# Optimization experiments

Hardware: AMD Instinct MI355X
Metric: run time of the kernel (lower is better)

Reference implementation:

```python
import jax, jax.numpy as jnp
import numpy as np

D_MODEL = 1024
D_STATE = 16
EXPANSION = 2
GROUPS = 16
D_INNER = EXPANSION * D_MODEL          # 2048
GROUP_SIZE = D_INNER // GROUPS         # 128
B, T = 2, 1024


def _rmsnorm(x, g, eps=1e-6):
    return x * jax.lax.rsqrt(jnp.mean(x * x, axis=-1, keepdims=True) + eps) * g


def setup_inputs() -> dict:
    key = jax.random.key(0)
    ks = jax.random.split(key, 8)
    s_in = 1.0 / np.sqrt(D_MODEL)
    s_inner = 1.0 / np.sqrt(D_INNER)
    s_ff = 1.0 / np.sqrt(4 * D_MODEL)
    return {
        "x": jax.random.normal(ks[0], (B, T, D_MODEL), dtype=jnp.float32),
        "A_log": jnp.log(jnp.linspace(1.0, float(D_STATE), D_STATE)).astype(jnp.float32),
        "g1": jnp.ones((D_MODEL,), jnp.float32),
        "g2": jnp.ones((D_MODEL,), jnp.float32),
        "W_in": jax.random.normal(ks[1], (2 * D_INNER, D_MODEL), jnp.float32) * s_in,
        "W_param": jax.random.normal(ks[2], (GROUPS * (1 + 2 * D_STATE), D_INNER), jnp.float32) * s_inner,
        "W_out": jax.random.normal(ks[3], (D_MODEL, D_INNER), jnp.float32) * s_inner,
        "W_ffn1": jax.random.normal(ks[4], (4 * D_MODEL, D_MODEL), jnp.float32) * s_in,
        "b_ffn1": jnp.zeros((4 * D_MODEL,), jnp.float32),
        "W_ffn2": jax.random.normal(ks[5], (D_MODEL, 4 * D_MODEL), jnp.float32) * s_ff,
        "b_ffn2": jnp.zeros((D_MODEL,), jnp.float32),
    }


def _ssm(u, delta, b, c, A_log):
    # u,delta: [B,T,D]; b,c: [B,T,D,N]. Sequential recurrence equivalent to
    # the module's chunked cumprod/cumsum formulation.
    A = -jnp.exp(A_log)                                   # [N]
    deltaA = jnp.clip(delta[..., None] * A, -10.0, 10.0)  # [B,T,D,N]
    expA = jnp.exp(deltaA)
    frac_exact = (expA - 1.0) / (A + 1e-12)
    frac = jnp.where(jnp.abs(deltaA) < 1e-4, delta[..., None], frac_exact)
    Bu = frac * (b * u[..., None])                        # [B,T,D,N]

    def step(h, inp):
        Ah_t, Bu_t, c_t = inp                             # [B,D,N] each
        h = Ah_t * h + Bu_t
        return h, jnp.sum(h * c_t, axis=-1)               # y_t: [B,D]

    tm = lambda a: jnp.moveaxis(a, 1, 0)                  # time-major [T,B,D,N]
    h0 = jnp.zeros(u.shape[:1] + u.shape[2:] + (A.shape[0],), u.dtype)
    _, ys = jax.lax.scan(step, h0, (tm(expA), tm(Bu), tm(c)))
    return jnp.moveaxis(ys, 0, 1)                         # [B,T,D]


def reference(x, A_log, g1, g2, W_in, W_param, W_out, W_ffn1, b_ffn1, W_ffn2, b_ffn2):
    Bsz, Tlen, _ = x.shape
    z = _rmsnorm(x, g1)
    xz_gate = jnp.einsum('btd,ed->bte', z, W_in)          # [B,T,2*D_inner]
    xz, gate = jnp.split(xz_gate, 2, axis=-1)
    xz = jax.nn.silu(xz)

    params = jnp.einsum('btd,pd->btp', xz, W_param)
    params = params.reshape(Bsz, Tlen, GROUPS, 1 + 2 * D_STATE)
    delta_g = params[..., :1]                             # [B,T,G,1]
    b_g = params[..., 1:1 + D_STATE]                      # [B,T,G,N]
    c_g = params[..., 1 + D_STATE:]                       # [B,T,G,N]
    delta = jax.nn.softplus(jnp.repeat(delta_g[..., 0], GROUP_SIZE, axis=2))  # [B,T,D_inner]
    b = jnp.repeat(b_g, GROUP_SIZE, axis=2)               # [B,T,D_inner,N]
    c = jnp.repeat(c_g, GROUP_SIZE, axis=2)

    y_ssm = _ssm(xz, delta, b, c, A_log)                  # [B,T,D_inner]
    y = y_ssm * jax.nn.silu(gate)
    y = jnp.einsum('bte,de->btd', y, W_out)
    x = x + y                                             # residual (dropout/droppath = identity in eval)

    h2 = _rmsnorm(x, g2)
    ffn = jnp.einsum('btf,df->btd',
                     jax.nn.silu(jnp.einsum('btd,fd->btf', h2, W_ffn1) + b_ffn1),
                     W_ffn2) + b_ffn2
    return x + ffn
```

## Files before the change

### kernel.cpp

```cpp
#include <hip/hip_runtime.h>
#include <hip/hip_bf16.h>
#include <stdint.h>

#define ROWS 2048
#define DM   1024
#define DI   2048
#define PPAD 640

typedef __bf16 bf16_t;
typedef __attribute__((ext_vector_type(8))) __bf16 bf16x8;
typedef __attribute__((ext_vector_type(4))) __bf16 bf16x4;
typedef __attribute__((ext_vector_type(4))) float f32x4;
typedef __attribute__((address_space(1))) void gvoid_t;
typedef __attribute__((address_space(3))) void lvoid_t;

#define G_IN   1048576ll
#define G_PAR  327680ll
#define G_OUT  524288ll
#define G_F1   1048576ll
#define G_F2   1048576ll
#define CVT_BLOCKS 15616
__global__ __launch_bounds__(256) void prep0(const float* __restrict__ W_in,
                                             const float* __restrict__ W_param,
                                             const float* __restrict__ W_out,
                                             const float* __restrict__ W_f1,
                                             const float* __restrict__ W_f2,
                                             bf16_t* o_in, bf16_t* o_par,
                                             bf16_t* o_out, bf16_t* o_f1,
                                             bf16_t* o_f2,
                                             const float* __restrict__ x,
                                             const float* __restrict__ g1,
                                             bf16_t* __restrict__ zb) {
  if (blockIdx.x >= CVT_BLOCKS) {
    int row = blockIdx.x - CVT_BLOCKS;
    int tid = threadIdx.x;
    const float4 v = *(const float4*)(x + (int64_t)row * DM + tid * 4);
    float ss = v.x * v.x + v.y * v.y + v.z * v.z + v.w * v.w;
#pragma unroll
    for (int o = 32; o; o >>= 1) ss += __shfl_xor(ss, o, 64);
    __shared__ float red[4];
    if ((tid & 63) == 0) red[tid >> 6] = ss;
    __syncthreads();
    float tot = red[0] + red[1] + red[2] + red[3];
    float sc = rsqrtf(tot * (1.0f / DM) + 1e-6f);
    const float4 gv = *(const float4*)(g1 + tid * 4);
    bf16_t* o = zb + (int64_t)row * DM + tid * 4;
    o[0] = (bf16_t)(v.x * sc * gv.x);
    o[1] = (bf16_t)(v.y * sc * gv.y);
    o[2] = (bf16_t)(v.z * sc * gv.z);
    o[3] = (bf16_t)(v.w * sc * gv.w);
    return;
  }
  int64_t g4 = (int64_t)blockIdx.x * 256 + threadIdx.x;
  const float* src; bf16_t* dst; int64_t e;
  if (g4 < G_IN) { e = g4 * 4; src = W_in; dst = o_in; }
  else if (g4 < G_IN + G_PAR) {
    e = (g4 - G_IN) * 4;
    int row = (int)(e >> 11), col = (int)(e & 2047);
    float4 v = make_float4(0.f, 0.f, 0.f, 0.f);
    if (row < 528) v = *(const float4*)(W_param + (int64_t)row * 2048 + col);
    bf16_t* o = o_par + e;
    o[0] = (bf16_t)v.x; o[1] = (bf16_t)v.y; o[2] = (bf16_t)v.z; o[3] = (bf16_t)v.w;
    return;
  }
  else if (g4 < G_IN + G_PAR + G_OUT) { e = (g4 - G_IN - G_PAR) * 4; src = W_out; dst = o_out; }
  else if (g4 < G_IN + G_PAR + G_OUT + G_F1) { e = (g4 - G_IN - G_PAR - G_OUT) * 4; src = W_f1; dst = o_f1; }
  else { e = (g4 - G_IN - G_PAR - G_OUT - G_F1) * 4; src = W_f2; dst = o_f2; }
  float4 v = *(const float4*)(src + e);
  bf16_t* o = dst + e;
  o[0] = (bf16_t)v.x; o[1] = (bf16_t)v.y; o[2] = (bf16_t)v.z; o[3] = (bf16_t)v.w;
}

__global__ __launch_bounds__(256) void rmsnorm_k(const float* __restrict__ x,
                                                 const float* __restrict__ g,
                                                 bf16_t* __restrict__ out) {
  int row = blockIdx.x;
  int tid = threadIdx.x;
  const float4 v = *(const float4*)(x + (int64_t)row * DM + tid * 4);
  float ss = v.x * v.x + v.y * v.y + v.z * v.z + v.w * v.w;
#pragma unroll
  for (int o = 32; o; o >>= 1) ss += __shfl_xor(ss, o, 64);
  __shared__ float red[4];
  if ((tid & 63) == 0) red[tid >> 6] = ss;
  __syncthreads();
  float tot = red[0] + red[1] + red[2] + red[3];
  float sc = rsqrtf(tot * (1.0f / DM) + 1e-6f);
  const float4 gv = *(const float4*)(g + tid * 4);
  bf16_t* o = out + (int64_t)row * DM + tid * 4;
  o[0] = (bf16_t)(v.x * sc * gv.x);
  o[1] = (bf16_t)(v.y * sc * gv.y);
  o[2] = (bf16_t)(v.z * sc * gv.z);
  o[3] = (bf16_t)(v.w * sc * gv.w);
}

__global__ __launch_bounds__(256) void silu_cvt(const float* __restrict__ in,
                                                bf16_t* __restrict__ out,
                                                int in_stride, int ncols) {
  int64_t e = ((int64_t)blockIdx.x * 256 + threadIdx.x) * 4;
  int row = (int)(e / ncols);
  int col = (int)(e % ncols);
  const float4 v = *(const float4*)(in + (int64_t)row * in_stride + col);
  bf16_t* o = out + e;
  o[0] = (bf16_t)(v.x / (1.f + expf(-v.x)));
  o[1] = (bf16_t)(v.y / (1.f + expf(-v.y)));
  o[2] = (bf16_t)(v.z / (1.f + expf(-v.z)));
  o[3] = (bf16_t)(v.w / (1.f + expf(-v.w)));
}

template <typename T>
__global__ __launch_bounds__(256) void ssm_prep(const T* __restrict__ params,
                                                const float* __restrict__ A_log,
                                                float* __restrict__ ssmp, int nparts) {
  int gid = blockIdx.x * 256 + threadIdx.x;
  int bg = gid >> 10, t = gid & 1023;
  int b = bg >> 4, g = bg & 15;
  float acc[33];
#pragma unroll
  for (int i = 0; i < 33; ++i) acc[i] = 0.f;
  for (int p = 0; p < nparts; ++p) {
    const T* pr = params + (int64_t)p * ROWS * PPAD + (int64_t)(b * 1024 + t) * PPAD + g * 33;
#pragma unroll
    for (int i = 0; i < 33; ++i) acc[i] += (float)pr[i];
  }
  float raw = acc[0];
  float delta = raw > 0.f ? raw + log1pf(expf(-raw)) : log1pf(expf(raw));
  float* o = ssmp + (int64_t)gid * 48;
#pragma unroll
  for (int s = 0; s < 16; ++s) {
    float A = -expf(A_log[s]);
    float dA = delta * A;
    dA = fminf(10.f, fmaxf(-10.f, dA));
    float e = expf(dA);
    float frac = (fabsf(dA) < 1e-4f) ? delta : (e - 1.f) / (A + 1e-12f);
    o[s] = dA;
    o[16 + s] = frac * acc[1 + s];
    o[32 + s] = acc[17 + s];
  }
}

__global__ __launch_bounds__(256) void reduce_rms(const bf16_t* __restrict__ P,
                                                  const float* __restrict__ x,
                                                  const float* __restrict__ g,
                                                  float* __restrict__ xmid,
                                                  bf16_t* __restrict__ zb) {
  int row = blockIdx.x;
  int tid = threadIdx.x;
  int64_t base = (int64_t)row * DM + tid * 4;
  float4 v = *(const float4*)(x + base);
#pragma unroll
  for (int p = 0; p < 4; ++p) {
    bf16x4 pv = *(const bf16x4*)(P + (int64_t)p * ROWS * DM + base);
    v.x += (float)pv[0]; v.y += (float)pv[1]; v.z += (float)pv[2]; v.w += (float)pv[3];
  }
  *(float4*)(xmid + base) = v;
  float ss = v.x * v.x + v.y * v.y + v.z * v.z + v.w * v.w;
#pragma unroll
  for (int o = 32; o; o >>= 1) ss += __shfl_xor(ss, o, 64);
  __shared__ float red[4];
  if ((tid & 63) == 0) red[tid >> 6] = ss;
  __syncthreads();
  float tot = red[0] + red[1] + red[2] + red[3];
  float sc = rsqrtf(tot * (1.0f / DM) + 1e-6f);
  const float4 gv = *(const float4*)(g + tid * 4);
  bf16_t* o = zb + base;
  o[0] = (bf16_t)(v.x * sc * gv.x);
  o[1] = (bf16_t)(v.y * sc * gv.y);
  o[2] = (bf16_t)(v.z * sc * gv.z);
  o[3] = (bf16_t)(v.w * sc * gv.w);
}

__global__ __launch_bounds__(256) void reduce_bias(const bf16_t* __restrict__ P,
                                                   const float* __restrict__ res,
                                                   const float* __restrict__ bias,
                                                   float* __restrict__ out) {
  int64_t e = ((int64_t)blockIdx.x * 256 + threadIdx.x) * 4;
  int col = (int)(e % DM);
  float4 v = *(const float4*)(res + e);
  const float4 bv = *(const float4*)(bias + col);
  v.x += bv.x; v.y += bv.y; v.z += bv.z; v.w += bv.w;
#pragma unroll
  for (int p = 0; p < 4; ++p) {
    bf16x4 pv = *(const bf16x4*)(P + (int64_t)p * ROWS * DM + e);
    v.x += (float)pv[0]; v.y += (float)pv[1]; v.z += (float)pv[2]; v.w += (float)pv[3];
  }
  *(float4*)(out + e) = v;
}


__global__ __launch_bounds__(256) void ssm_chunk(const float* __restrict__ ssmp,
                                                 const bf16_t* __restrict__ u,
                                                 float* __restrict__ S,
                                                 float* __restrict__ Etot) {
  __shared__ __align__(16) float cf[64 * 48];
  __shared__ __align__(16) float Lb[64 * 16];
  __shared__ __align__(16) bf16_t wl[16 * 64];
  __shared__ __align__(16) bf16_t Ut[128 * 64];
  int bgc = blockIdx.x;
  int bg = bgc >> 4, c = bgc & 15;
  int b = bg >> 4, g = bg & 15;
  int t0 = c * 64;
  int tid = threadIdx.x;
  {
    const float4* src = (const float4*)(ssmp + ((int64_t)bg * 1024 + t0) * 48);
    float4* dst = (float4*)cf;
#pragma unroll
    for (int i = 0; i < 3; ++i) dst[i * 256 + tid] = src[i * 256 + tid];
  }
  {
    int lt = tid >> 4;
    int c8 = (tid & 15) * 8;
#pragma unroll
    for (int p = 0; p < 4; ++p) {
      int t = p * 16 + lt;
      bf16x8 v = *(const bf16x8*)(u + ((int64_t)(b * 1024) + t0 + t) * 2048 + g * 128 + c8);
#pragma unroll
      for (int j = 0; j < 8; ++j)
        Ut[(c8 + j) * 64 + (((t >> 3) ^ j) << 3) + (t & 7)] = v[j];
    }
  }
  __syncthreads();
  if (tid < 16) {
    float l = 0.f;
    for (int t = 0; t < 64; ++t) { l += cf[t * 48 + tid]; Lb[t * 16 + tid] = l; }
  }
  __syncthreads();
  {
    int s = tid >> 4, tb4 = (tid & 15) * 4;
    float lend = Lb[63 * 16 + s];
    bf16x4 wv;
#pragma unroll
    for (int j = 0; j < 4; ++j) {
      int t = tb4 + j;
      wv[j] = (bf16_t)(__expf(lend - Lb[t * 16 + s]) * cf[t * 48 + 16 + s]);
    }
    unsigned byo = (unsigned)(s * 128 + tb4 * 2) ^ ((unsigned)(s & 7) << 4);
    *(bf16x4*)((char*)wl + byo) = wv;
    if (tid < 16) Etot[(int64_t)bgc * 16 + tid] = __expf(Lb[63 * 16 + tid]);
  }
  __syncthreads();
  {
    int lane = tid & 63, wave = tid >> 6;
    int fr = lane & 15, kq = lane >> 4;
    f32x4 acc2[2] = {};
#pragma unroll
    for (int kk = 0; kk < 2; ++kk) {
      int kb = kk * 4 + kq;
      bf16x8 af = *(const bf16x8*)((const char*)wl +
                    ((unsigned)(fr * 128 + kb * 16) ^ ((unsigned)(fr & 7) << 4)));
#pragma unroll
      for (int q = 0; q < 2; ++q) {
        int ch = (wave * 2 + q) * 16 + fr;
        bf16x8 bfr = *(const bf16x8*)((const char*)Ut +
                       ((unsigned)(ch * 128 + kb * 16) ^ ((unsigned)(ch & 7) << 4)));
        acc2[q] = __builtin_amdgcn_mfma_f32_16x16x32_bf16(af, bfr, acc2[q], 0, 0, 0);
      }
    }
    float* Sp = S + (int64_t)bgc * 2048;
#pragma unroll
    for (int q = 0; q < 2; ++q) {
      int ch = (wave * 2 + q) * 16 + fr;
#pragma unroll
      for (int j = 0; j < 4; ++j) Sp[(kq * 4 + j) * 128 + ch] = acc2[q][j];
    }
  }
}

__global__ __launch_bounds__(256) void ssm_combine(const float* __restrict__ S,
                                                   const float* __restrict__ Etot,
                                                   float* __restrict__ H) {
  int gid = blockIdx.x * 256 + threadIdx.x;
  int bg = gid >> 11;
  int s = (gid >> 7) & 15;
  int ch = gid & 127;
  float h = 0.f;
  for (int c = 0; c < 16; ++c) {
    int bgc = bg * 16 + c;
    int64_t idx = ((int64_t)bgc * 16 + s) * 128 + ch;
    H[idx] = h;
    h = Etot[(int64_t)bgc * 16 + s] * h + S[idx];
  }
}

template <int GM>
__global__ __launch_bounds__(256) void ssm_out(const float* __restrict__ ssmp,
                                               const bf16_t* __restrict__ u,
                                               const float* __restrict__ H,
                                               const float* __restrict__ gate_f,
                                               const bf16_t* __restrict__ gate_b,
                                               int gstride,
                                               bf16_t* __restrict__ yout) {
  __shared__ __align__(16) float cf[64 * 48];
  __shared__ __align__(16) float Lb[64 * 16];
  __shared__ __align__(16) bf16_t Km[64 * 64];
  __shared__ __align__(16) bf16_t Ut[128 * 64];
  __shared__ __align__(16) bf16_t Hb[128 * 32];
  int bgc = blockIdx.x;
  int bg = bgc >> 4, c = bgc & 15;
  int b = bg >> 4, g = bg & 15;
  int t0 = c * 64;
  int tid = threadIdx.x;
  int lane = tid & 63, wave = tid >> 6;
  {
    const float4* src = (const float4*)(ssmp + ((int64_t)bg * 1024 + t0) * 48);
    float4* dst = (float4*)cf;
#pragma unroll
    for (int i = 0; i < 3; ++i) dst[i * 256 + tid] = src[i * 256 + tid];
  }
  {
    int lt = tid >> 4;
    int c8 = (tid & 15) * 8;
#pragma unroll
    for (int p = 0; p < 4; ++p) {
      int t = p * 16 + lt;
      bf16x8 v = *(const bf16x8*)(u + ((int64_t)(b * 1024) + t0 + t) * 2048 + g * 128 + c8);
#pragma unroll
      for (int j = 0; j < 8; ++j)
        Ut[(c8 + j) * 64 + (((t >> 3) ^ j) << 3) + (t & 7)] = v[j];
    }
  }
  {
    int ch = tid >> 1, h8 = (tid & 1) * 8;
    const float* Hp = H + (int64_t)bgc * 2048 + ch;
#pragma unroll
    for (int j = 0; j < 8; ++j) {
      Hb[ch * 32 + h8 + j] = (bf16_t)Hp[(h8 + j) * 128];
      Hb[ch * 32 + 16 + h8 + j] = (bf16_t)0.f;
    }
  }
  __syncthreads();
  if (tid < 16) {
    float l = 0.f;
    for (int t = 0; t < 64; ++t) { l += cf[t * 48 + tid]; Lb[t * 16 + tid] = l; }
  }
  __syncthreads();
  {
    int t = tid >> 2, tp0 = (tid & 3) * 16;
    float4 cv[4], lv[4];
#pragma unroll
    for (int i = 0; i < 4; ++i) {
      cv[i] = *(const float4*)&cf[t * 48 + 32 + i * 4];
      lv[i] = *(const float4*)&Lb[t * 16 + i * 4];
    }
    float kv[16];
#pragma unroll
    for (int i = 0; i < 16; ++i) {
      int tp = tp0 + i;
      float k = 0.f;
      if (tp <= t) {
#pragma unroll
        for (int q = 0; q < 4; ++q) {
          float4 lpv = *(const float4*)&Lb[tp * 16 + q * 4];
          float4 fbv = *(const float4*)&cf[tp * 48 + 16 + q * 4];
          k += cv[q].x * __expf(lv[q].x - lpv.x) * fbv.x
             + cv[q].y * __expf(lv[q].y - lpv.y) * fbv.y
             + cv[q].z * __expf(lv[q].z - lpv.z) * fbv.z
             + cv[q].w * __expf(lv[q].w - lpv.w) * fbv.w;
        }
      }
      kv[i] = k;
    }
    bf16x8 lo, hi;
#pragma unroll
    for (int i = 0; i < 8; ++i) { lo[i] = (bf16_t)kv[i]; hi[i] = (bf16_t)kv[8 + i]; }
    unsigned b0 = (unsigned)(t * 128 + tp0 * 2) ^ ((unsigned)(t & 7) << 4);
    unsigned b1 = (unsigned)(t * 128 + tp0 * 2 + 16) ^ ((unsigned)(t & 7) << 4);
    *(bf16x8*)((char*)Km + b0) = lo;
    *(bf16x8*)((char*)Km + b1) = hi;
  }
  __syncthreads();
  int fr = lane & 15, kq = lane >> 4;
  int trow = (wave >> 1) * 32, wc = (wave & 1) * 64;
  f32x4 acc[2][4] = {};
#pragma unroll
  for (int kk = 0; kk < 2; ++kk) {
    int kb = kk * 4 + kq;
    bf16x8 af[2];
#pragma unroll
    for (int mi = 0; mi < 2; ++mi) {
      int row = trow + mi * 16 + fr;
      af[mi] = *(const bf16x8*)((const char*)Km +
                 ((unsigned)(row * 128 + kb * 16) ^ ((unsigned)(row & 7) << 4)));
    }
#pragma unroll
    for (int ni = 0; ni < 4; ++ni) {
      int ch = wc + ni * 16 + fr;
      bf16x8 bfr = *(const bf16x8*)((const char*)Ut +
                     ((unsigned)(ch * 128 + kb * 16) ^ ((unsigned)(ch & 7) << 4)));
#pragma unroll
      for (int mi = 0; mi < 2; ++mi)
        acc[mi][ni] = __builtin_amdgcn_mfma_f32_16x16x32_bf16(af[mi], bfr, acc[mi][ni], 0, 0, 0);
    }
  }
  {
    int s0 = kq * 8;
    bf16x8 cef[2];
    if (s0 < 16) {
#pragma unroll
      for (int mi = 0; mi < 2; ++mi) {
        int t = trow + mi * 16 + fr;
#pragma unroll
        for (int j = 0; j < 8; ++j)
          cef[mi][j] = (bf16_t)(cf[t * 48 + 32 + s0 + j] * __expf(Lb[t * 16 + s0 + j]));
      }
    } else {
#pragma unroll
      for (int mi = 0; mi < 2; ++mi)
#pragma unroll
        for (int j = 0; j < 8; ++j) cef[mi][j] = (bf16_t)0.f;
    }
#pragma unroll
    for (int ni = 0; ni < 4; ++ni) {
      int ch = wc + ni * 16 + fr;
      bf16x8 bhf = *(const bf16x8*)((const char*)Hb + ch * 64 + s0 * 2);
#pragma unroll
      for (int mi = 0; mi < 2; ++mi)
        acc[mi][ni] = __builtin_amdgcn_mfma_f32_16x16x32_bf16(cef[mi], bhf, acc[mi][ni], 0, 0, 0);
    }
  }
  {
    int64_t rowbase = (int64_t)b * 1024 + t0;
    int colbase = g * 128;
#pragma unroll
    for (int mi = 0; mi < 2; ++mi) {
#pragma unroll
      for (int ni = 0; ni < 4; ++ni) {
        int col = colbase + wc + ni * 16 + fr;
#pragma unroll
        for (int j = 0; j < 4; ++j) {
          int t = trow + mi * 16 + kq * 4 + j;
          float sg;
          if (GM) {
            sg = (float)gate_b[(rowbase + t) * 2048 + col];
          } else {
            float gv = gate_f[(rowbase + t) * (int64_t)gstride + col];
            sg = gv / (1.f + __expf(-gv));
          }
          yout[(rowbase + t) * 2048 + col] = (bf16_t)(acc[mi][ni][j] * sg);
        }
      }
    }
  }
}

template <int EPI>
__device__ __forceinline__ void epi_store(float v, int64_t r, int64_t cn, int N,
                                          float* Cz, const float* bias,
                                          const float* res, bf16_t* obf,
                                          bf16_t* ogate, int z) {
  if (EPI & 1) v += bias[cn];
  if (EPI & 2) v += res[r * N + cn];
  if (EPI & 4) {
    float sv = v / (1.f + __expf(-v));
    if (cn < 2048) obf[r * 2048 + cn] = (bf16_t)sv;
    else ogate[r * 2048 + cn - 2048] = (bf16_t)sv;
  } else if (EPI & 8) {
    obf[r * N + cn] = (bf16_t)(v / (1.f + __expf(-v)));
  } else if (EPI & 16) {
    obf[(int64_t)z * ROWS * N + r * N + cn] = (bf16_t)v;
  } else {
    Cz[r * N + cn] = v;
  }
}

__device__ __forceinline__ void xcd_swz(int& bx, int& by, int& bz) {
  int gx = gridDim.x, gy = gridDim.y, gz = gridDim.z;
  int flat = blockIdx.x + gx * (blockIdx.y + gy * blockIdx.z);
  int nwg = gx * gy * gz;
  int swz = flat;
  if ((nwg & 7) == 0) swz = (flat & 7) * (nwg >> 3) + (flat >> 3);
  bx = swz % gx;
  int rem = swz / gx;
  by = rem % gy;
  bz = rem / gy;
}

template <int EPI>
__global__ __launch_bounds__(256) void gemm_bt(const bf16_t* __restrict__ A,
                                               const bf16_t* __restrict__ Bw,
                                               float* __restrict__ C,
                                               const float* __restrict__ bias,
                                               const float* __restrict__ res,
                                               bf16_t* __restrict__ obf,
                                               bf16_t* __restrict__ ogate,
                                               int N, int Kps) {
  __shared__ bf16_t As[2][128 * 64];
  __shared__ bf16_t Bs[2][128 * 64];
  const int tid = threadIdx.x;
  const int wave = tid >> 6;
  const int lane = tid & 63;
  int bxi, byi, bzi;
  xcd_swz(bxi, byi, bzi);
  const int64_t m0 = (int64_t)byi * 128;
  const int64_t n0 = (int64_t)bxi * 128;
  const int K = Kps * gridDim.z;
  const int kbeg = bzi * Kps;
  float* Cz = C + (int64_t)bzi * ROWS * N;
  const int wm = (wave >> 1) * 64;
  const int wn = (wave & 1) * 64;
  f32x4 acc[4][4] = {};

  const int er = tid >> 3;
  const int ec = (tid * 8) & 63;
  const int fr = lane & 15;
  const int kq = (lane >> 4) * 8;

  auto stage = [&](int buf, int k0) {
#pragma unroll
    for (int i = 0; i < 4; ++i) {
      const bf16_t* ga = A + (m0 + er + i * 32) * K + k0 + ec;
      __builtin_amdgcn_global_load_lds((gvoid_t*)ga,
                                       (lvoid_t*)&As[buf][(i * 256 + wave * 64) * 8],
                                       16, 0, 0);
    }
#pragma unroll
    for (int i = 0; i < 4; ++i) {
      const bf16_t* gb = Bw + (n0 + er + i * 32) * K + k0 + ec;
      __builtin_amdgcn_global_load_lds((gvoid_t*)gb,
                                       (lvoid_t*)&Bs[buf][(i * 256 + wave * 64) * 8],
                                       16, 0, 0);
    }
  };
  auto compute = [&](int buf) {
#pragma unroll
    for (int kk = 0; kk < 2; ++kk) {
      bf16x8 af[4], bv[4];
#pragma unroll
      for (int mi = 0; mi < 4; ++mi)
        af[mi] = *reinterpret_cast<const bf16x8*>(&As[buf][(wm + mi * 16 + fr) * 64 + kk * 32 + kq]);
#pragma unroll
      for (int ni = 0; ni < 4; ++ni)
        bv[ni] = *reinterpret_cast<const bf16x8*>(&Bs[buf][(wn + ni * 16 + fr) * 64 + kk * 32 + kq]);
#pragma unroll
      for (int mi = 0; mi < 4; ++mi)
#pragma unroll
        for (int ni = 0; ni < 4; ++ni)
          acc[mi][ni] = __builtin_amdgcn_mfma_f32_16x16x32_bf16(af[mi], bv[ni], acc[mi][ni], 0, 0, 0);
    }
  };

  const int nk = Kps >> 6;
  stage(0, kbeg);
  asm volatile("s_waitcnt vmcnt(0)" ::: "memory");
  __builtin_amdgcn_s_barrier();
  int kc = kbeg;
  for (int t = 0; t < nk; t += 2) {
    stage(1, kc + 64);
    compute(0);
    asm volatile("s_waitcnt vmcnt(0)" ::: "memory");
    __builtin_amdgcn_s_barrier();
    if (t + 2 < nk) stage(0, kc + 128);
    compute(1);
    asm volatile("s_waitcnt vmcnt(0)" ::: "memory");
    __builtin_amdgcn_s_barrier();
    kc += 128;
  }

  const int crow = (lane >> 4) * 4;
  const int ccol = lane & 15;
#pragma unroll
  for (int mi = 0; mi < 4; ++mi)
#pragma unroll
    for (int ni = 0; ni < 4; ++ni)
#pragma unroll
      for (int j = 0; j < 4; ++j)
        epi_store<EPI>(acc[mi][ni][j], m0 + wm + mi * 16 + crow + j,
                       n0 + wn + ni * 16 + ccol, N, Cz, bias, res, obf, ogate,
                       bzi);
}

template <int EPI>
__global__ __launch_bounds__(512, 2) void gemm_big(const bf16_t* __restrict__ A,
                                                   const bf16_t* __restrict__ Bw,
                                                   float* __restrict__ C,
                                                   const float* __restrict__ bias,
                                                   const float* __restrict__ res,
                                                   bf16_t* __restrict__ obf,
                                                   bf16_t* __restrict__ ogate,
                                                   int N, int Kps) {
  __shared__ bf16_t As[2][128 * 64];
  __shared__ bf16_t Bs[2][256 * 64];
  const int tid = threadIdx.x;
  const int wave = tid >> 6;
  const int lane = tid & 63;
  int bxi, byi, bzi;
  xcd_swz(bxi, byi, bzi);
  const int64_t m0 = (int64_t)byi * 128;
  const int64_t n0 = (int64_t)bxi * 256;
  const int K = Kps * gridDim.z;
  const int kbeg = bzi * Kps;
  float* Cz = C + (int64_t)bzi * ROWS * N;
  const int wm = (wave >> 2) * 64;
  const int wc = (wave & 3) * 64;
  const int fr = lane & 15;
  const int kq16 = (lane >> 4) * 16;
  const int er = tid >> 3;
  const int ec_sw = ((tid & 7) * 8) ^ ((er & 7) << 3);
  f32x4 acc[4][4] = {};

  auto stage = [&](int buf, int k0) {
#pragma unroll
    for (int i = 0; i < 2; ++i) {
      const bf16_t* ga = A + (m0 + er + i * 64) * K + k0 + ec_sw;
      __builtin_amdgcn_global_load_lds((gvoid_t*)ga,
          (lvoid_t*)((char*)&As[buf][0] + i * 8192 + wave * 1024), 16, 0, 0);
    }
#pragma unroll
    for (int i = 0; i < 4; ++i) {
      const bf16_t* gb = Bw + (n0 + er + i * 64) * K + k0 + ec_sw;
      __builtin_amdgcn_global_load_lds((gvoid_t*)gb,
          (lvoid_t*)((char*)&Bs[buf][0] + i * 8192 + wave * 1024), 16, 0, 0);
    }
  };

  const int nk = Kps >> 6;
  stage(0, kbeg);
  if (nk > 1) {
    stage(1, kbeg + 64);
    asm volatile("s_waitcnt vmcnt(6)" ::: "memory");
  } else {
    asm volatile("s_waitcnt vmcnt(0)" ::: "memory");
  }
  __builtin_amdgcn_s_barrier();
  __builtin_amdgcn_sched_barrier(0);

  for (int t = 0; t < nk; ++t) {
    const int buf = t & 1;
    bf16x8 af[2][4], bf[2][4];
#pragma unroll
    for (int kk = 0; kk < 2; ++kk) {
#pragma unroll
      for (int mi = 0; mi < 4; ++mi) {
        int r = wm + mi * 16 + fr;
        af[kk][mi] = *(const bf16x8*)((const char*)&As[buf][0] + r * 128 +
                       ((kk * 64 + kq16) ^ ((r & 7) << 4)));
      }
#pragma unroll
      for (int ni = 0; ni < 4; ++ni) {
        int r = wc + ni * 16 + fr;
        bf[kk][ni] = *(const bf16x8*)((const char*)&Bs[buf][0] + r * 128 +
                       ((kk * 64 + kq16) ^ ((r & 7) << 4)));
      }
    }
    asm volatile("s_waitcnt lgkmcnt(8)" ::: "memory");
    __builtin_amdgcn_sched_barrier(0);
    __builtin_amdgcn_s_setprio(1);
#pragma unroll
    for (int mi = 0; mi < 4; ++mi)
#pragma unroll
      for (int ni = 0; ni < 4; ++ni)
        acc[mi][ni] = __builtin_amdgcn_mfma_f32_16x16x32_bf16(
            af[0][mi], bf[0][ni], acc[mi][ni], 0, 0, 0);
    __builtin_amdgcn_s_setprio(0);
    __builtin_amdgcn_sched_barrier(0);
    asm volatile("s_waitcnt lgkmcnt(0)" ::: "memory");
    __builtin_amdgcn_sched_barrier(0);
    __builtin_amdgcn_s_barrier();
    __builtin_amdgcn_sched_barrier(0);
    if (t + 2 < nk) stage(buf, kbeg + (t + 2) * 64);
    __builtin_amdgcn_s_setprio(1);
#pragma unroll
    for (int mi = 0; mi < 4; ++mi)
#pragma unroll
      for (int ni = 0; ni < 4; ++ni)
        acc[mi][ni] = __builtin_amdgcn_mfma_f32_16x16x32_bf16(
            af[1][mi], bf[1][ni], acc[mi][ni], 0, 0, 0);
    __builtin_amdgcn_s_setprio(0);
    if (t + 1 < nk) {
      if (t + 2 < nk) asm volatile("s_waitcnt vmcnt(6)" ::: "memory");
      else            asm volatile("s_waitcnt vmcnt(0)" ::: "memory");
      __builtin_amdgcn_s_barrier();
      __builtin_amdgcn_sched_barrier(0);
    }
  }

  const int crow = (lane >> 4) * 4;
  const int ccol = lane & 15;
#pragma unroll
  for (int mi = 0; mi < 4; ++mi)
#pragma unroll
    for (int ni = 0; ni < 4; ++ni)
#pragma unroll
      for (int j = 0; j < 4; ++j)
        epi_store<EPI>(acc[mi][ni][j], m0 + wm + mi * 16 + crow + j,
                       n0 + wc + ni * 16 + ccol, N, Cz, bias, res, obf, ogate,
                       bzi);
}

extern "C" void kernel_launch(void* const* d_in, const int* in_sizes, int n_in,
                              void* d_out, int out_size, void* d_ws, size_t ws_size,
                              hipStream_t stream) {
  const float* x       = (const float*)d_in[0];
  const float* A_log   = (const float*)d_in[1];
  const float* g1      = (const float*)d_in[2];
  const float* g2      = (const float*)d_in[3];
  const float* W_in    = (const float*)d_in[4];
  const float* W_param = (const float*)d_in[5];
  const float* W_out   = (const float*)d_in[6];
  const float* W_ffn1  = (const float*)d_in[7];
  const float* b_ffn1  = (const float*)d_in[8];
  const float* W_ffn2  = (const float*)d_in[9];
  const float* b_ffn2  = (const float*)d_in[10];
  float* out = (float*)d_out;

  char* ws = (char*)d_ws;
  size_t off = 0;
  auto alloc = [&](size_t bytes) {
    char* p = ws + off;
    off += (bytes + 255) & ~(size_t)255;
    return p;
  };
  bf16_t* wb_in  = (bf16_t*)alloc(4096ull * 1024 * 2);
  bf16_t* wb_par = (bf16_t*)alloc((size_t)PPAD * 2048 * 2);
  bf16_t* wb_out = (bf16_t*)alloc(1024ull * 2048 * 2);
  bf16_t* wb_f1  = (bf16_t*)alloc(4096ull * 1024 * 2);
  bf16_t* wb_f2  = (bf16_t*)alloc(1024ull * 4096 * 2);
  bf16_t* zbuf   = (bf16_t*)alloc(2048ull * 1024 * 2);
  float*  xzg    = (float*)alloc(2048ull * 4096 * 4);
  float*  params = (float*)alloc(2048ull * PPAD * 4);
  float*  ssmp   = (float*)alloc(32ull * 1024 * 48 * 4);
  float*  xmid   = (float*)alloc(2048ull * 1024 * 4);
  char*   regA   = alloc(2048ull * 4096 * 2);
  bf16_t* xz_act = (bf16_t*)regA;
  bf16_t* y_b16  = (bf16_t*)(regA + 2048ull * 2048 * 2);
  bf16_t* f_act  = (bf16_t*)regA;
  bf16_t* sgate  = (bf16_t*)xzg;
  float* Sbuf = params;
  float* Etot = params + 32ull * 16 * 16 * 128;
  float* Hbuf = xmid;
  float*  psum = (float*)alloc(4ull * ROWS * 1024 * 4);
  bf16_t* pb16 = (bf16_t*)psum;
  const bool sk = (off <= ws_size);

  dim3 b256(256), b512(512);
  prep0<<<CVT_BLOCKS + 2048, b256, 0, stream>>>(W_in, W_param, W_out, W_ffn1, W_ffn2,
                                                wb_in, wb_par, wb_out, wb_f1, wb_f2,
                                                x, g1, zbuf);

  if (sk) {
    gemm_big<4><<<dim3(16, 16), b512, 0, stream>>>(zbuf, wb_in, psum, nullptr, nullptr, xz_act, sgate, 4096, 1024);
    gemm_bt<16><<<dim3(PPAD / 128, 16, 4), b256, 0, stream>>>(xz_act, wb_par, psum, nullptr, nullptr, pb16, nullptr, PPAD, 512);
    ssm_prep<bf16_t><<<128, b256, 0, stream>>>(pb16, A_log, ssmp, 4);
    ssm_chunk<<<512, b256, 0, stream>>>(ssmp, xz_act, Sbuf, Etot);
    ssm_combine<<<256, b256, 0, stream>>>(Sbuf, Etot, Hbuf);
    ssm_out<1><<<512, b256, 0, stream>>>(ssmp, xz_act, Hbuf, nullptr, sgate, 2048, y_b16);
    gemm_big<16><<<dim3(4, 16, 4), b512, 0, stream>>>(y_b16, wb_out, psum, nullptr, nullptr, pb16, nullptr, 1024, 512);
    reduce_rms<<<2048, b256, 0, stream>>>(pb16, x, g2, xmid, zbuf);
    gemm_big<9><<<dim3(16, 16), b512, 0, stream>>>(zbuf, wb_f1, psum, b_ffn1, nullptr, f_act, nullptr, 4096, 1024);
    gemm_big<16><<<dim3(4, 16, 4), b512, 0, stream>>>(f_act, wb_f2, psum, nullptr, nullptr, pb16, nullptr, 1024, 1024);
    reduce_bias<<<2048, b256, 0, stream>>>(pb16, xmid, b_ffn2, out);
  } else {
    gemm_bt<0><<<dim3(32, 16), b256, 0, stream>>>(zbuf, wb_in, xzg, nullptr, nullptr, nullptr, nullptr, 4096, 1024);
    silu_cvt<<<4096, b256, 0, stream>>>(xzg, xz_act, 4096, 2048);
    gemm_bt<0><<<dim3(PPAD / 128, 16), b256, 0, stream>>>(xz_act, wb_par, params, nullptr, nullptr, nullptr, nullptr, PPAD, 2048);
    ssm_prep<float><<<128, b256, 0, stream>>>(params, A_log, ssmp, 1);
    ssm_chunk<<<512, b256, 0, stream>>>(ssmp, xz_act, Sbuf, Etot);
    ssm_combine<<<256, b256, 0, stream>>>(Sbuf, Etot, Hbuf);
    ssm_out<0><<<512, b256, 0, stream>>>(ssmp, xz_act, Hbuf, xzg + 2048, nullptr, 4096, y_b16);
    gemm_bt<2><<<dim3(8, 16), b256, 0, stream>>>(y_b16, wb_out, xmid, nullptr, x, nullptr, nullptr, 1024, 2048);
    rmsnorm_k<<<2048, b256, 0, stream>>>(xmid, g2, zbuf);
    gemm_bt<1><<<dim3(32, 16), b256, 0, stream>>>(zbuf, wb_f1, xzg, b_ffn1, nullptr, nullptr, nullptr, 4096, 1024);
    silu_cvt<<<8192, b256, 0, stream>>>(xzg, f_act, 4096, 4096);
    gemm_bt<3><<<dim3(8, 16), b256, 0, stream>>>(f_act, wb_f2, out, b_ffn2, xmid, nullptr, nullptr, 1024, 4096);
  }
}
```

Baseline: 188.6 us.

## Overlap late weight conversion with param GEMM and fuse ssm_prep into SSM kernels

After: 176.8 us. 1.07x faster.

```diff
diff --git a/kernel.cpp b/kernel.cpp
--- a/kernel.cpp
+++ b/kernel.cpp
@@ -14,26 +14,15 @@
 typedef __attribute__((address_space(1))) void gvoid_t;
 typedef __attribute__((address_space(3))) void lvoid_t;
 
-#define G_IN   1048576ll
-#define G_PAR  327680ll
-#define G_OUT  524288ll
-#define G_F1   1048576ll
-#define G_F2   1048576ll
-#define CVT_BLOCKS 15616
 __global__ __launch_bounds__(256) void prep0(const float* __restrict__ W_in,
                                              const float* __restrict__ W_param,
-                                             const float* __restrict__ W_out,
-                                             const float* __restrict__ W_f1,
-                                             const float* __restrict__ W_f2,
                                              bf16_t* o_in, bf16_t* o_par,
-                                             bf16_t* o_out, bf16_t* o_f1,
-                                             bf16_t* o_f2,
                                              const float* __restrict__ x,
                                              const float* __restrict__ g1,
                                              bf16_t* __restrict__ zb) {
-  if (blockIdx.x >= CVT_BLOCKS) {
-    int row = blockIdx.x - CVT_BLOCKS;
-    int tid = threadIdx.x;
+  int tid = threadIdx.x;
+  if (blockIdx.x >= 5376) {
+    int row = blockIdx.x - 5376;
     const float4 v = *(const float4*)(x + (int64_t)row * DM + tid * 4);
     float ss = v.x * v.x + v.y * v.y + v.z * v.z + v.w * v.w;
 #pragma unroll
@@ -51,11 +40,8 @@
     o[3] = (bf16_t)(v.w * sc * gv.w);
     return;
   }
-  int64_t g4 = (int64_t)blockIdx.x * 256 + threadIdx.x;
-  const float* src; bf16_t* dst; int64_t e;
-  if (g4 < G_IN) { e = g4 * 4; src = W_in; dst = o_in; }
-  else if (g4 < G_IN + G_PAR) {
-    e = (g4 - G_IN) * 4;
+  if (blockIdx.x >= 4096) {
+    int64_t e = (((int64_t)(blockIdx.x - 4096)) * 256 + tid) * 4;
     int row = (int)(e >> 11), col = (int)(e & 2047);
     float4 v = make_float4(0.f, 0.f, 0.f, 0.f);
     if (row < 528) v = *(const float4*)(W_param + (int64_t)row * 2048 + col);
@@ -63,12 +49,32 @@
     o[0] = (bf16_t)v.x; o[1] = (bf16_t)v.y; o[2] = (bf16_t)v.z; o[3] = (bf16_t)v.w;
     return;
   }
-  else if (g4 < G_IN + G_PAR + G_OUT) { e = (g4 - G_IN - G_PAR) * 4; src = W_out; dst = o_out; }
-  else if (g4 < G_IN + G_PAR + G_OUT + G_F1) { e = (g4 - G_IN - G_PAR - G_OUT) * 4; src = W_f1; dst = o_f1; }
-  else { e = (g4 - G_IN - G_PAR - G_OUT - G_F1) * 4; src = W_f2; dst = o_f2; }
+  int64_t e = ((int64_t)blockIdx.x * 256 + tid) * 4;
+  float4 v = *(const float4*)(W_in + e);
+  bf16_t* o = o_in + e;
+  o[0] = (bf16_t)v.x; o[1] = (bf16_t)v.y; o[2] = (bf16_t)v.z; o[3] = (bf16_t)v.w;
+}
+
+__device__ __forceinline__ void conv3(int64_t c, int tid,
+                                      const float* __restrict__ W_out,
+                                      const float* __restrict__ W_f1,
+                                      const float* __restrict__ W_f2,
+                                      bf16_t* o_out, bf16_t* o_f1, bf16_t* o_f2) {
+  const float* src; bf16_t* dst; int64_t e;
+  if (c < 2048) { e = (c * 256 + tid) * 4; src = W_out; dst = o_out; }
+  else if (c < 6144) { e = ((c - 2048) * 256 + tid) * 4; src = W_f1; dst = o_f1; }
+  else { e = ((c - 6144) * 256 + tid) * 4; src = W_f2; dst = o_f2; }
   float4 v = *(const float4*)(src + e);
   bf16_t* o = dst + e;
   o[0] = (bf16_t)v.x; o[1] = (bf16_t)v.y; o[2] = (bf16_t)v.z; o[3] = (bf16_t)v.w;
+}
+
+__global__ __launch_bounds__(256) void cvt3_k(const float* __restrict__ W_out,
+                                              const float* __restrict__ W_f1,
+                                              const float* __restrict__ W_f2,
+                                              bf16_t* o_out, bf16_t* o_f1,
+                                              bf16_t* o_f2) {
+  conv3(blockIdx.x, threadIdx.x, W_out, W_f1, W_f2, o_out, o_f1, o_f2);
 }
 
 __global__ __launch_bounds__(256) void rmsnorm_k(const float* __restrict__ x,
@@ -107,22 +113,14 @@
   o[3] = (bf16_t)(v.w / (1.f + expf(-v.w)));
 }
 
-template <typename T>
-__global__ __launch_bounds__(256) void ssm_prep(const T* __restrict__ params,
+__global__ __launch_bounds__(256) void ssm_prep(const float* __restrict__ params,
                                                 const float* __restrict__ A_log,
-                                                float* __restrict__ ssmp, int nparts) {
+                                                float* __restrict__ ssmp) {
   int gid = blockIdx.x * 256 + threadIdx.x;
   int bg = gid >> 10, t = gid & 1023;
   int b = bg >> 4, g = bg & 15;
-  float acc[33];
-#pragma unroll
-  for (int i = 0; i < 33; ++i) acc[i] = 0.f;
-  for (int p = 0; p < nparts; ++p) {
-    const T* pr = params + (int64_t)p * ROWS * PPAD + (int64_t)(b * 1024 + t) * PPAD + g * 33;
-#pragma unroll
-    for (int i = 0; i < 33; ++i) acc[i] += (float)pr[i];
-  }
-  float raw = acc[0];
+  const float* pr = params + (int64_t)(b * 1024 + t) * PPAD + g * 33;
+  float raw = pr[0];
   float delta = raw > 0.f ? raw + log1pf(expf(-raw)) : log1pf(expf(raw));
   float* o = ssmp + (int64_t)gid * 48;
 #pragma unroll
@@ -133,8 +131,8 @@
     float e = expf(dA);
     float frac = (fabsf(dA) < 1e-4f) ? delta : (e - 1.f) / (A + 1e-12f);
     o[s] = dA;
-    o[16 + s] = frac * acc[1 + s];
-    o[32 + s] = acc[17 + s];
+    o[16 + s] = frac * pr[1 + s];
+    o[32 + s] = pr[17 + s];
   }
 }
 
@@ -186,8 +184,43 @@
   *(float4*)(out + e) = v;
 }
 
-
+__device__ __forceinline__ void prep_rows(const bf16_t* __restrict__ pb,
+                                          const float* __restrict__ A_log,
+                                          float* cf, int b, int g, int t0,
+                                          int tid) {
+  if (tid >= 64) return;
+  int t = tid;
+  int64_t row = (int64_t)(b * 1024) + t0 + t;
+  float acc[33];
+#pragma unroll
+  for (int i = 0; i < 33; ++i) acc[i] = 0.f;
+#pragma unroll
+  for (int p = 0; p < 4; ++p) {
+    const bf16_t* pr = pb + (int64_t)p * ROWS * PPAD + row * PPAD + g * 33;
+#pragma unroll
+    for (int i = 0; i < 33; ++i) acc[i] += (float)pr[i];
+  }
+  float raw = acc[0];
+  float delta = raw > 0.f ? raw + log1pf(expf(-raw)) : log1pf(expf(raw));
+  float* o = cf + t * 48;
+#pragma unroll
+  for (int s = 0; s < 16; ++s) {
+    float A = -expf(A_log[s]);
+    float dA = delta * A;
+    dA = fminf(10.f, fmaxf(-10.f, dA));
+    float e = expf(dA);
+    float frac = (fabsf(dA) < 1e-4f) ? delta : (e - 1.f) / (A + 1e-12f);
+    o[s] = dA;
+    o[16 + s] = frac * acc[1 + s];
+    o[32 + s] = acc[17 + s];
+  }
+}
+
+
+template <int PREP>
 __global__ __launch_bounds__(256) void ssm_chunk(const float* __restrict__ ssmp,
+                                                 const bf16_t* __restrict__ pb,
+                                                 const float* __restrict__ A_log,
                                                  const bf16_t* __restrict__ u,
                                                  float* __restrict__ S,
                                                  float* __restrict__ Etot) {
@@ -201,12 +234,6 @@
   int t0 = c * 64;
   int tid = threadIdx.x;
   {
-    const float4* src = (const float4*)(ssmp + ((int64_t)bg * 1024 + t0) * 48);
-    float4* dst = (float4*)cf;
-#pragma unroll
-    for (int i = 0; i < 3; ++i) dst[i * 256 + tid] = src[i * 256 + tid];
-  }
-  {
     int lt = tid >> 4;
     int c8 = (tid & 15) * 8;
 #pragma unroll
@@ -217,6 +244,14 @@
       for (int j = 0; j < 8; ++j)
         Ut[(c8 + j) * 64 + (((t >> 3) ^ j) << 3) + (t & 7)] = v[j];
     }
+  }
+  if (PREP) {
+    prep_rows(pb, A_log, cf, b, g, t0, tid);
+  } else {
+    const float4* src = (const float4*)(ssmp + ((int64_t)bg * 1024 + t0) * 48);
+    float4* dst = (float4*)cf;
+#pragma unroll
+    for (int i = 0; i < 3; ++i) dst[i * 256 + tid] = src[i * 256 + tid];
   }
   __syncthreads();
   if (tid < 16) {
@@ -281,8 +316,10 @@
   }
 }
 
-template <int GM>
+template <int PREP, int GM>
 __global__ __launch_bounds__(256) void ssm_out(const float* __restrict__ ssmp,
+                                               const bf16_t* __restrict__ pb,
+                                               const float* __restrict__ A_log,
                                                const bf16_t* __restrict__ u,
                                                const float* __restrict__ H,
                                                const float* __restrict__ gate_f,
@@ -301,12 +338,6 @@
   int tid = threadIdx.x;
   int lane = tid & 63, wave = tid >> 6;
   {
-    const float4* src = (const float4*)(ssmp + ((int64_t)bg * 1024 + t0) * 48);
-    float4* dst = (float4*)cf;
-#pragma unroll
-    for (int i = 0; i < 3; ++i) dst[i * 256 + tid] = src[i * 256 + tid];
-  }
-  {
     int lt = tid >> 4;
     int c8 = (tid & 15) * 8;
 #pragma unroll
@@ -326,6 +357,14 @@
       Hb[ch * 32 + h8 + j] = (bf16_t)Hp[(h8 + j) * 128];
       Hb[ch * 32 + 16 + h8 + j] = (bf16_t)0.f;
     }
+  }
+  if (PREP) {
+    prep_rows(pb, A_log, cf, b, g, t0, tid);
+  } else {
+    const float4* src = (const float4*)(ssmp + ((int64_t)bg * 1024 + t0) * 48);
+    float4* dst = (float4*)cf;
+#pragma unroll
+    for (int i = 0; i < 3; ++i) dst[i * 256 + tid] = src[i * 256 + tid];
   }
   __syncthreads();
   if (tid < 16) {
@@ -566,6 +605,104 @@
         epi_store<EPI>(acc[mi][ni][j], m0 + wm + mi * 16 + crow + j,
                        n0 + wn + ni * 16 + ccol, N, Cz, bias, res, obf, ogate,
                        bzi);
+}
+
+__global__ __launch_bounds__(256) void gemm_param_conv(
+    const bf16_t* __restrict__ A, const bf16_t* __restrict__ Bw,
+    bf16_t* __restrict__ pout,
+    const float* __restrict__ W_out, const float* __restrict__ W_f1,
+    const float* __restrict__ W_f2,
+    bf16_t* o_out, bf16_t* o_f1, bf16_t* o_f2) {
+  __shared__ bf16_t As[2][128 * 64];
+  __shared__ bf16_t Bs[2][128 * 64];
+  const int tid = threadIdx.x;
+  if (blockIdx.x >= 320) {
+    conv3(blockIdx.x - 320, tid, W_out, W_f1, W_f2, o_out, o_f1, o_f2);
+    return;
+  }
+  const int flat = blockIdx.x;
+  const int swz = (flat & 7) * 40 + (flat >> 3);
+  const int bxi = swz % 5;
+  const int byi = (swz / 5) % 16;
+  const int bzi = swz / 80;
+  const int wave = tid >> 6;
+  const int lane = tid & 63;
+  const int64_t m0 = (int64_t)byi * 128;
+  const int64_t n0 = (int64_t)bxi * 128;
+  const int K = 2048, Kps = 512;
+  const int kbeg = bzi * Kps;
+  const int wm = (wave >> 1) * 64;
+  const int wn = (wave & 1) * 64;
+  f32x4 acc[4][4] = {};
+  const int er = tid >> 3;
+  const int ec = (tid * 8) & 63;
+  const int fr = lane & 15;
+  const int kq = (lane >> 4) * 8;
+
+  auto stage = [&](int buf, int k0) {
+#pragma unroll
+    for (int i = 0; i < 4; ++i) {
+      const bf16_t* ga = A + (m0 + er + i * 32) * K + k0 + ec;
+      __builtin_amdgcn_global_load_lds((gvoid_t*)ga,
+                                       (lvoid_t*)&As[buf][(i * 256 + wave * 64) * 8],
+                                       16, 0, 0);
+    }
+#pragma unroll
+    for (int i = 0; i < 4; ++i) {
+      const bf16_t* gb = Bw + (n0 + er + i * 32) * K + k0 + ec;
+      __builtin_amdgcn_global_load_lds((gvoid_t*)gb,
+                                       (lvoid_t*)&Bs[buf][(i * 256 + wave * 64) * 8],
+                                       16, 0, 0);
+    }
+  };
+  auto compute = [&](int buf) {
+#pragma unroll
+    for (int kk = 0; kk < 2; ++kk) {
+      bf16x8 af[4], bv[4];
+#pragma unroll
+      for (int mi = 0; mi < 4; ++mi)
+        af[mi] = *reinterpret_cast<const bf16x8*>(&As[buf][(wm + mi * 16 + fr) * 64 + kk * 32 + kq]);
+#pragma unroll
+      for (int ni = 0; ni < 4; ++ni)
+        bv[ni] = *reinterpret_cast<const bf16x8*>(&Bs[buf][(wn + ni * 16 + fr) * 64 + kk * 32 + kq]);
+#pragma unroll
+      for (int mi = 0; mi < 4; ++mi)
+#pragma unroll
+        for (int ni = 0; ni < 4; ++ni)
+          acc[mi][ni] = __builtin_amdgcn_mfma_f32_16x16x32_bf16(af[mi], bv[ni], acc[mi][ni], 0, 0, 0);
+    }
+  };
+
+  const int nk = Kps >> 6;
+  stage(0, kbeg);
+  asm volatile("s_waitcnt vmcnt(0)" ::: "memory");
+  __builtin_amdgcn_s_barrier();
+  int kc = kbeg;
+  for (int t = 0; t < nk; t += 2) {
+    stage(1, kc + 64);
+    compute(0);
+    asm volatile("s_waitcnt vmcnt(0)" ::: "memory");
+    __builtin_amdgcn_s_barrier();
+    if (t + 2 < nk) stage(0, kc + 128);
+    compute(1);
+    asm volatile("s_waitcnt vmcnt(0)" ::: "memory");
+    __builtin_amdgcn_s_barrier();
+    kc += 128;
+  }
+
+  const int crow = (lane >> 4) * 4;
+  const int ccol = lane & 15;
+  bf16_t* pz = pout + (int64_t)bzi * ROWS * PPAD;
+#pragma unroll
+  for (int mi = 0; mi < 4; ++mi)
+#pragma unroll
+    for (int ni = 0; ni < 4; ++ni)
+#pragma unroll
+      for (int j = 0; j < 4; ++j) {
+        int64_t r = m0 + wm + mi * 16 + crow + j;
+        int64_t cn = n0 + wn + ni * 16 + ccol;
+        pz[r * PPAD + cn] = (bf16_t)acc[mi][ni][j];
+      }
 }
 
 template <int EPI>
@@ -732,30 +869,30 @@
   const bool sk = (off <= ws_size);
 
   dim3 b256(256), b512(512);
-  prep0<<<CVT_BLOCKS + 2048, b256, 0, stream>>>(W_in, W_param, W_out, W_ffn1, W_ffn2,
-                                                wb_in, wb_par, wb_out, wb_f1, wb_f2,
-                                                x, g1, zbuf);
+  prep0<<<7424, b256, 0, stream>>>(W_in, W_param, wb_in, wb_par, x, g1, zbuf);
 
   if (sk) {
     gemm_big<4><<<dim3(16, 16), b512, 0, stream>>>(zbuf, wb_in, psum, nullptr, nullptr, xz_act, sgate, 4096, 1024);
-    gemm_bt<16><<<dim3(PPAD / 128, 16, 4), b256, 0, stream>>>(xz_act, wb_par, psum, nullptr, nullptr, pb16, nullptr, PPAD, 512);
-    ssm_prep<bf16_t><<<128, b256, 0, stream>>>(pb16, A_log, ssmp, 4);
-    ssm_chunk<<<512, b256, 0, stream>>>(ssmp, xz_act, Sbuf, Etot);
+    gemm_param_conv<<<10560, b256, 0, stream>>>(xz_act, wb_par, pb16,
+                                                W_out, W_ffn1, W_ffn2,
+                                                wb_out, wb_f1, wb_f2);
+    ssm_chunk<1><<<512, b256, 0, stream>>>(nullptr, pb16, A_log, xz_act, Sbuf, Etot);
     ssm_combine<<<256, b256, 0, stream>>>(Sbuf, Etot, Hbuf);
-    ssm_out<1><<<512, b256, 0, stream>>>(ssmp, xz_act, Hbuf, nullptr, sgate, 2048, y_b16);
+    ssm_out<1, 1><<<512, b256, 0, stream>>>(nullptr, pb16, A_log, xz_act, Hbuf, nullptr, sgate, 2048, y_b16);
     gemm_big<16><<<dim3(4, 16, 4), b512, 0, stream>>>(y_b16, wb_out, psum, nullptr, nullptr, pb16, nullptr, 1024, 512);
     reduce_rms<<<2048, b256, 0, stream>>>(pb16, x, g2, xmid, zbuf);
     gemm_big<9><<<dim3(16, 16), b512, 0, stream>>>(zbuf, wb_f1, psum, b_ffn1, nullptr, f_act, nullptr, 4096, 1024);
     gemm_big<16><<<dim3(4, 16, 4), b512, 0, stream>>>(f_act, wb_f2, psum, nullptr, nullptr, pb16, nullptr, 1024, 1024);
     reduce_bias<<<2048, b256, 0, stream>>>(pb16, xmid, b_ffn2, out);
   } else {
+    cvt3_k<<<10240, b256, 0, stream>>>(W_out, W_ffn1, W_ffn2, wb_out, wb_f1, wb_f2);
     gemm_bt<0><<<dim3(32, 16), b256, 0, stream>>>(zbuf, wb_in, xzg, nullptr, nullptr, nullptr, nullptr, 4096, 1024);
     silu_cvt<<<4096, b256, 0, stream>>>(xzg, xz_act, 4096, 2048);
     gemm_bt<0><<<dim3(PPAD / 128, 16), b256, 0, stream>>>(xz_act, wb_par, params, nullptr, nullptr, nullptr, nullptr, PPAD, 2048);
-    ssm_prep<float><<<128, b256, 0, stream>>>(params, A_log, ssmp, 1);
-    ssm_chunk<<<512, b256, 0, stream>>>(ssmp, xz_act, Sbuf, Etot);
+    ssm_prep<<<128, b256, 0, stream>>>(params, A_log, ssmp);
+    ssm_chunk<0><<<512, b256, 0, stream>>>(ssmp, nullptr, A_log, xz_act, Sbuf, Etot);
     ssm_combine<<<256, b256, 0, stream>>>(Sbuf, Etot, Hbuf);
-    ssm_out<0><<<512, b256, 0, stream>>>(ssmp, xz_act, Hbuf, xzg + 2048, nullptr, 4096, y_b16);
+    ssm_out<0, 0><<<512, b256, 0, stream>>>(ssmp, nullptr, A_log, xz_act, Hbuf, xzg + 2048, nullptr, 4096, y_b16);
     gemm_bt<2><<<dim3(8, 16), b256, 0, stream>>>(y_b16, wb_out, xmid, nullptr, x, nullptr, nullptr, 1024, 2048);
     rmsnorm_k<<<2048, b256, 0, stream>>>(xmid, g2, zbuf);
     gemm_bt<1><<<dim3(32, 16), b256, 0, stream>>>(zbuf, wb_f1, xzg, b_ffn1, nullptr, nullptr, nullptr, 4096, 1024);
```
